# Performance work log

Measured on AMD Instinct MI355X. Metric: run time of the kernel, lower is better.

## Reference

```python
import jax, jax.numpy as jnp
import numpy as np

K = 3          # involution kernel size
GROUPS = 32    # channels == GROUPS * K*K
BN_EPS = 1e-5

def _conv1x1(x, W, b):
    # x: (B,C,H,W), W: (Co,C), b: (Co,)
    return jnp.einsum('bchw,oc->bohw', x, W) + b[None, :, None, None]

def setup_inputs() -> dict:
    key = jax.random.key(0)
    ks = jax.random.split(key, 5)
    C = GROUPS * K * K  # 288
    x = jax.random.normal(ks[0], (8, C, 64, 64), dtype=jnp.float32)
    Wi = jax.random.normal(ks[1], (C, C), dtype=jnp.float32) * 0.05
    bi = jnp.zeros((C,), dtype=jnp.float32)
    gamma = jnp.ones((C,), dtype=jnp.float32)
    beta = jnp.zeros((C,), dtype=jnp.float32)
    Wo = jax.random.normal(ks[2], (C, C), dtype=jnp.float32) * 0.05
    bo = jnp.zeros((C,), dtype=jnp.float32)
    return {"x": x, "Wi": Wi, "bi": bi, "gamma": gamma, "beta": beta, "Wo": Wo, "bo": bo}

def reference(x, Wi, bi, gamma, beta, Wo, bo):
    B, C, H, W = x.shape
    # kernel generation branch (stride=1 -> avgpool is identity)
    tmp = jax.nn.relu(_conv1x1(x, Wi, bi))
    # BatchNorm2d in training mode: batch stats over (N,H,W), biased variance
    mean = jnp.mean(tmp, axis=(0, 2, 3), keepdims=True)
    var = jnp.var(tmp, axis=(0, 2, 3), keepdims=True)
    tmp = (tmp - mean) * jax.lax.rsqrt(var + BN_EPS)
    tmp = tmp * gamma[None, :, None, None] + beta[None, :, None, None]
    ker = _conv1x1(tmp, Wo, bo)                       # (B, G*K^2, H, W)
    ker = ker.reshape(B, GROUPS, K * K, H, W)         # (B, G, K^2, H, W)
    # unfold: extract KxK patches with padding (K-1)//2, stride 1
    p = (K - 1) // 2
    xp = jnp.pad(x, ((0, 0), (0, 0), (p, p), (p, p)))
    patches = jnp.stack(
        [xp[:, :, i:i + H, j:j + W] for i in range(K) for j in range(K)],
        axis=2,
    )  # (B, C, K^2, H, W), kernel-position minor — matches torch unfold layout
    patches = patches.reshape(B, GROUPS, C // GROUPS, K * K, H, W)
    # per-pixel dynamic kernel multiply + sum over kernel positions
    out = jnp.einsum('bgkhw,bgckhw->bgchw', ker, patches)
    return out.reshape(B, C, H, W)
```

## Files before the change

### kernel.cpp

```cpp
#include <hip/hip_runtime.h>

#define CH   288
#define GRPS 32
#define CPG  9
#define IMH  64
#define IMW  64
#define HW   4096
#define NB   8
#define NPX  (NB * HW)
#define BN_EPS 1e-5f

typedef short bf16x8 __attribute__((ext_vector_type(8)));
typedef float f32x4  __attribute__((ext_vector_type(4)));

#define XT_OFF   0u
#define WIB_OFF  18874368u
#define WOS_OFF  19040256u
#define S1_OFF   19206144u
#define S2_OFF   19207296u
#define SC_OFF   19208448u
#define SH_OFF   19209600u
#define BO2_OFF  19210752u

#define XB 36864
#define WB 18432

__device__ __forceinline__ unsigned short f2b(float f) {
    unsigned int u = __float_as_uint(f);
    return (unsigned short)((u + 0x7fffu + ((u >> 16) & 1u)) >> 16);
}
__device__ __forceinline__ float b2f(unsigned short h) {
    return __uint_as_float(((unsigned int)h) << 16);
}

#define GLDS(g, l) __builtin_amdgcn_global_load_lds( \
    (const __attribute__((address_space(1))) void*)(g), \
    (__attribute__((address_space(3))) void*)(l), 16, 0, 0)

__device__ __forceinline__ f32x4 mfma16(bf16x8 a, bf16x8 b, f32x4 c) {
    return __builtin_amdgcn_mfma_f32_16x16x32_bf16(a, b, c, 0, 0, 0);
}

#define TS 40
__global__ __launch_bounds__(256) void k_transpose(const float* __restrict__ x,
                                                   unsigned short* __restrict__ xt) {
    __shared__ unsigned short T[64 * TS];
    const int tid = threadIdx.x;
    const int p0 = blockIdx.x * 64;
    const int c0 = blockIdx.y * 32;
    const int b  = blockIdx.z;
    #pragma unroll
    for (int it = 0; it < 2; ++it) {
        const int item  = it * 256 + tid;
        const int c_loc = item >> 4;
        const int p4    = item & 15;
        const float4 v = *(const float4*)(x + (size_t)(b * CH + c0 + c_loc) * HW + p0 + p4 * 4);
        const int px = p4 * 4;
        T[(px + 0) * TS + c_loc] = f2b(v.x);
        T[(px + 1) * TS + c_loc] = f2b(v.y);
        T[(px + 2) * TS + c_loc] = f2b(v.z);
        T[(px + 3) * TS + c_loc] = f2b(v.w);
    }
    __syncthreads();
    const int px_loc = tid >> 2;
    const int cq     = tid & 3;
    const uint4 o = *(const uint4*)((const char*)T + px_loc * (TS * 2) + cq * 16);
    *(uint4*)(xt + ((size_t)b * HW + p0 + px_loc) * CH + c0 + cq * 8) = o;
}

__global__ __launch_bounds__(256) void k_cvt_wi(const float* __restrict__ Wi,
                                                unsigned short* __restrict__ Wib) {
    const int idx = blockIdx.x * 256 + threadIdx.x;
    const float4 v = ((const float4*)Wi)[idx];
    unsigned short h[4] = {f2b(v.x), f2b(v.y), f2b(v.z), f2b(v.w)};
    *(uint2*)(Wib + (size_t)idx * 4) = *(const uint2*)h;
}

#define GEMM_STEP(KK, WBASE) do {                                              \
    bf16x8 xf0, xf1;                                                           \
    { const int row0 = pxh * 32 + r;                                           \
      xf0 = *(const bf16x8*)(smc + row0 * 576 + (KK) * 64 +                    \
                             ((q ^ ((row0 >> 1) & 3)) * 16)); }                \
    { const int row1 = pxh * 32 + 16 + r;                                      \
      xf1 = *(const bf16x8*)(smc + row1 * 576 + (KK) * 64 +                    \
                             ((q ^ ((row1 >> 1) & 3)) * 16)); }                \
    _Pragma("unroll")                                                          \
    for (int j = 0; j < 9; ++j) {                                              \
        const int ro = chh * 144 + j * 16 + r;                                 \
        const bf16x8 wf = *(const bf16x8*)((WBASE) + ro * 64 +                 \
                             ((q ^ ((ro >> 1) & 3)) * 16));                    \
        acc[0][j] = mfma16(wf, xf0, acc[0][j]);                                \
        acc[1][j] = mfma16(wf, xf1, acc[1][j]);                                \
    }                                                                          \
} while (0)

#define STAGE_W(WSRC, K0v, WDST) do {                                          \
    for (int s = wave; s < 18; s += 4) {                                       \
        const int row = s * 16 + lrow;                                         \
        const int sc  = lp ^ ((row >> 1) & 3);                                 \
        GLDS((WSRC) + (size_t)row * CH + (K0v) + sc * 8, (WDST) + s * 1024);   \
    }                                                                          \
} while (0)

#define STAGE_X(XSRC) do {                                                     \
    for (int s = wave; s < 36; s += 4) {                                       \
        const int d   = s * 1024 + lane * 16;                                  \
        const int px  = d / 576;                                               \
        const int rem = d - px * 576;                                          \
        const int kc  = rem >> 6;                                              \
        const int ch  = (rem >> 4) & 3;                                        \
        const int sc  = ch ^ ((px >> 1) & 3);                                  \
        GLDS((XSRC) + (size_t)px * CH + kc * 32 + sc * 8, smc + s * 1024);     \
    }                                                                          \
} while (0)

__global__ __launch_bounds__(256) void k_gemm1(const unsigned short* __restrict__ Wib,
                                               const float* __restrict__ bi,
                                               unsigned short* __restrict__ xt,
                                               float* __restrict__ s1g) {
    __shared__ char smc[XB + 2 * WB];

    const int tid  = threadIdx.x;
    const int wave = tid >> 6;
    const int lane = tid & 63;
    const int q    = lane >> 4;
    const int r    = lane & 15;
    const int pxh  = wave & 1;
    const int chh  = wave >> 1;
    const int p0   = blockIdx.x * 64;
    const int lrow = lane >> 2;
    const int lp   = lane & 3;

    f32x4 acc[2][9];
    #pragma unroll
    for (int t = 0; t < 2; ++t)
        #pragma unroll
        for (int j = 0; j < 9; ++j) acc[t][j] = (f32x4)0.0f;

    STAGE_X(xt + (size_t)p0 * CH);
    STAGE_W(Wib, 0, smc + XB);
    asm volatile("s_waitcnt vmcnt(0)" ::: "memory");
    __builtin_amdgcn_s_barrier();

    #pragma unroll 1
    for (int kk = 0; kk < 8; ++kk) {
        char* wnext = smc + XB + ((kk + 1) & 1) * WB;
        STAGE_W(Wib, (kk + 1) * 32, wnext);
        asm volatile("s_waitcnt vmcnt(4)" ::: "memory");
        __builtin_amdgcn_s_barrier();
        char* wcur = smc + XB + (kk & 1) * WB;
        GEMM_STEP(kk, wcur);
        __builtin_amdgcn_s_barrier();
    }
    asm volatile("s_waitcnt vmcnt(0)" ::: "memory");
    __builtin_amdgcn_s_barrier();
    GEMM_STEP(8, smc + XB);
    __syncthreads();

    float* sstat = (float*)(smc + 18432);
    for (int c2 = tid; c2 < 576; c2 += 256) sstat[c2] = 0.0f;
    __syncthreads();

    #pragma unroll 1
    for (int j = 0; j < 9; ++j) {
        const int cb = chh * 144 + j * 16 + q * 4;
        const float4 b4 = *(const float4*)(bi + cb);
        float a1[4] = {0.f, 0.f, 0.f, 0.f}, a2[4] = {0.f, 0.f, 0.f, 0.f};
        #pragma unroll
        for (int t = 0; t < 2; ++t) {
            float v0 = fmaxf(acc[t][j][0] + b4.x, 0.0f);
            float v1 = fmaxf(acc[t][j][1] + b4.y, 0.0f);
            float v2 = fmaxf(acc[t][j][2] + b4.z, 0.0f);
            float v3 = fmaxf(acc[t][j][3] + b4.w, 0.0f);
            a1[0] += v0; a1[1] += v1; a1[2] += v2; a1[3] += v3;
            a2[0] += v0 * v0; a2[1] += v1 * v1; a2[2] += v2 * v2; a2[3] += v3 * v3;
        }
        #pragma unroll
        for (int m = 1; m < 16; m <<= 1) {
            #pragma unroll
            for (int i = 0; i < 4; ++i) {
                a1[i] += __shfl_xor(a1[i], m, 64);
                a2[i] += __shfl_xor(a2[i], m, 64);
            }
        }
        if (r == 0) {
            #pragma unroll
            for (int i = 0; i < 4; ++i) {
                atomicAdd(&sstat[cb + i], a1[i]);
                atomicAdd(&sstat[288 + cb + i], a2[i]);
            }
        }
    }

    #pragma unroll
    for (int ph = 0; ph < 2; ++ph) {
        const int lr = pxh * 16 + r;
        #pragma unroll
        for (int j = 0; j < 9; ++j) {
            const int cb = chh * 144 + j * 16 + q * 4;
            const float4 b4 = *(const float4*)(bi + cb);
            unsigned short h[4];
            h[0] = f2b(fmaxf(acc[ph][j][0] + b4.x, 0.0f));
            h[1] = f2b(fmaxf(acc[ph][j][1] + b4.y, 0.0f));
            h[2] = f2b(fmaxf(acc[ph][j][2] + b4.z, 0.0f));
            h[3] = f2b(fmaxf(acc[ph][j][3] + b4.w, 0.0f));
            *(uint2*)(smc + lr * 576 + cb * 2) = *(const uint2*)h;
        }
        __syncthreads();
        for (int idx = tid; idx < 1152; idx += 256) {
            const int row = idx / 36;
            const int off = idx - row * 36;
            const int gpx = p0 + ph * 16 + row + (row & 16);
            *(uint4*)(xt + (size_t)gpx * CH + off * 8) =
                *(const uint4*)(smc + row * 576 + off * 16);
        }
        if (ph == 0) {
            for (int c2 = tid; c2 < 576; c2 += 256)
                atomicAdd(&s1g[c2], sstat[c2]);
        }
        __syncthreads();
    }
}

__global__ __launch_bounds__(320) void k_scale(const float* __restrict__ s1,
                                               const float* __restrict__ s2,
                                               const float* __restrict__ gamma,
                                               const float* __restrict__ beta,
                                               float* __restrict__ scale,
                                               float* __restrict__ shift) {
    const int c = threadIdx.x;
    if (c < CH) {
        const float inv = 1.0f / (float)(NB * HW);
        const float mean = s1[c] * inv;
        const float var  = s2[c] * inv - mean * mean;
        const float rs   = rsqrtf(var + BN_EPS);
        const float sc   = gamma[c] * rs;
        scale[c] = sc;
        shift[c] = beta[c] - mean * sc;
    }
}

__global__ __launch_bounds__(64) void k_fold(const float* __restrict__ Wo,
                                             const float* __restrict__ bo,
                                             const float* __restrict__ scale,
                                             const float* __restrict__ shift,
                                             unsigned short* __restrict__ Wos,
                                             float* __restrict__ bo2) {
    const int m = blockIdx.x;
    const int t = threadIdx.x;
    float s = 0.0f;
    for (int k = t; k < CH; k += 64) {
        const float wv = Wo[(size_t)m * CH + k];
        s += wv * shift[k];
        Wos[(size_t)m * CH + k] = f2b(wv * scale[k]);
    }
    #pragma unroll
    for (int off = 32; off > 0; off >>= 1) s += __shfl_down(s, off, 64);
    if (t == 0) bo2[m] = bo[m] + s;
}

#define KLS2 68
__global__ __launch_bounds__(256) void k_gemm2_invol(const unsigned short* __restrict__ xt,
                                                     const unsigned short* __restrict__ Wos,
                                                     const float* __restrict__ bo2,
                                                     const float* __restrict__ x,
                                                     float* __restrict__ out) {
    __shared__ char smc[XB + 2 * WB];
    unsigned short* kerL = (unsigned short*)smc;

    const int tid  = threadIdx.x;
    const int wave = tid >> 6;
    const int lane = tid & 63;
    const int q    = lane >> 4;
    const int r    = lane & 15;
    const int pxh  = wave & 1;
    const int chh  = wave >> 1;
    const int p0   = blockIdx.x * 64;
    const int b    = blockIdx.y;
    const int h    = blockIdx.x;
    const size_t rowbase = (size_t)b * HW + p0;
    const int lrow = lane >> 2;
    const int lp   = lane & 3;

    f32x4 acc[2][9];
    #pragma unroll
    for (int t = 0; t < 2; ++t)
        #pragma unroll
        for (int j = 0; j < 9; ++j) acc[t][j] = (f32x4)0.0f;

    STAGE_X(xt + rowbase * CH);
    STAGE_W(Wos, 0, smc + XB);
    asm volatile("s_waitcnt vmcnt(0)" ::: "memory");
    __builtin_amdgcn_s_barrier();

    #pragma unroll 1
    for (int kk = 0; kk < 8; ++kk) {
        char* wnext = smc + XB + ((kk + 1) & 1) * WB;
        STAGE_W(Wos, (kk + 1) * 32, wnext);
        asm volatile("s_waitcnt vmcnt(4)" ::: "memory");
        __builtin_amdgcn_s_barrier();
        char* wcur = smc + XB + (kk & 1) * WB;
        GEMM_STEP(kk, wcur);
        __builtin_amdgcn_s_barrier();
    }
    asm volatile("s_waitcnt vmcnt(0)" ::: "memory");
    __builtin_amdgcn_s_barrier();
    GEMM_STEP(8, smc + XB);
    __syncthreads();

    #pragma unroll
    for (int j = 0; j < 9; ++j) {
        const int cb = chh * 144 + j * 16 + q * 4;
        const float4 bz = *(const float4*)(bo2 + cb);
        #pragma unroll
        for (int t = 0; t < 2; ++t) {
            const int pxl = pxh * 32 + t * 16 + r;
            kerL[(cb + 0) * KLS2 + pxl] = f2b(acc[t][j][0] + bz.x);
            kerL[(cb + 1) * KLS2 + pxl] = f2b(acc[t][j][1] + bz.y);
            kerL[(cb + 2) * KLS2 + pxl] = f2b(acc[t][j][2] + bz.z);
            kerL[(cb + 3) * KLS2 + pxl] = f2b(acc[t][j][3] + bz.w);
        }
    }
    __syncthreads();

    const int tm = tid >> 4;
    const int tn = tid & 15;
    const int wb = tn * 4;
    #pragma unroll 1
    for (int i = 0; i < 18; ++i) {
        const int ch = tm + 16 * i;
        const int cb = (ch / CPG) * CPG;
        float xv[3][6];
        #pragma unroll
        for (int dr = 0; dr < 3; ++dr) {
            const int hh = h + dr - 1;
            const bool rv = (hh >= 0) && (hh < IMH);
            const float* xr2 = x + ((size_t)(b * CH + ch) * IMH + (rv ? hh : 0)) * IMW;
            if (rv) {
                const float4 m4 = *(const float4*)(xr2 + wb);
                xv[dr][1] = m4.x; xv[dr][2] = m4.y; xv[dr][3] = m4.z; xv[dr][4] = m4.w;
                xv[dr][0] = (wb > 0)       ? xr2[wb - 1] : 0.0f;
                xv[dr][5] = (wb + 4 < IMW) ? xr2[wb + 4] : 0.0f;
            } else {
                #pragma unroll
                for (int j = 0; j < 6; ++j) xv[dr][j] = 0.0f;
            }
        }
        float o[4] = {0.0f, 0.0f, 0.0f, 0.0f};
        #pragma unroll
        for (int k = 0; k < 9; ++k) {
            const int dr = k / 3, dc = k % 3;
            const uint2 kk = *(const uint2*)(kerL + (cb + k) * KLS2 + tn * 4);
            const unsigned short* ks = (const unsigned short*)&kk;
            #pragma unroll
            for (int j = 0; j < 4; ++j)
                o[j] += b2f(ks[j]) * xv[dr][j + dc];
        }
        float4 ov = {o[0], o[1], o[2], o[3]};
        *(float4*)(out + ((size_t)(b * CH + ch) * IMH + h) * IMW + wb) = ov;
    }
}

extern "C" void kernel_launch(void* const* d_in, const int* in_sizes, int n_in,
                              void* d_out, int out_size, void* d_ws, size_t ws_size,
                              hipStream_t stream) {
    const float* x     = (const float*)d_in[0];
    const float* Wi    = (const float*)d_in[1];
    const float* bi    = (const float*)d_in[2];
    const float* gamma = (const float*)d_in[3];
    const float* beta  = (const float*)d_in[4];
    const float* Wo    = (const float*)d_in[5];
    const float* bo    = (const float*)d_in[6];
    float* out = (float*)d_out;

    char* ws = (char*)d_ws;
    unsigned short* xt  = (unsigned short*)(ws + XT_OFF);
    unsigned short* Wib = (unsigned short*)(ws + WIB_OFF);
    unsigned short* Wos = (unsigned short*)(ws + WOS_OFF);
    float* s1    = (float*)(ws + S1_OFF);
    float* s2    = (float*)(ws + S2_OFF);
    float* scale = (float*)(ws + SC_OFF);
    float* shift = (float*)(ws + SH_OFF);
    float* bo2   = (float*)(ws + BO2_OFF);

    k_transpose<<<dim3(HW / 64, CH / 32, NB), 256, 0, stream>>>(x, xt);
    k_cvt_wi<<<dim3(CH * CH / 1024), 256, 0, stream>>>(Wi, Wib);
    hipMemsetAsync(ws + S1_OFF, 0, 2 * CH * sizeof(float), stream);
    k_gemm1<<<dim3(NPX / 64), 256, 0, stream>>>(Wib, bi, xt, s1);
    k_scale<<<dim3(1), 320, 0, stream>>>(s1, s2, gamma, beta, scale, shift);
    k_fold<<<dim3(CH), 64, 0, stream>>>(Wo, bo, scale, shift, Wos, bo2);
    k_gemm2_invol<<<dim3(HW / 64, NB), 256, 0, stream>>>(xt, Wos, bo2, x, out);
}
```

Before: 186.5 us.

## Shrink GEMM tiles, stream X with W per k-step, and spread BN-stat atomics over slots

gemm1 now processes 32 pixels per block instead of 64, with half the accumulators and launch_bounds(256,4), so more blocks can be resident per CU. Both GEMMs now stream X tiles k-slice by k-slice together with the weights instead of staging the full X tile up front, which shrinks LDS use. The global batch-norm atomics are spread over 64 slot buffers, which reuse the Wos workspace region, and k_scale reduces across the slots. This trades more blocks and extra X traffic per k-step for higher occupancy and less atomic contention, and it depends on k_fold overwriting the slot region afterwards.

```diff
diff --git a/kernel.cpp b/kernel.cpp
--- a/kernel.cpp
+++ b/kernel.cpp
@@ -9,6 +9,7 @@
 #define NB   8
 #define NPX  (NB * HW)
 #define BN_EPS 1e-5f
+#define NSLOT 64
 
 typedef short bf16x8 __attribute__((ext_vector_type(8)));
 typedef float f32x4  __attribute__((ext_vector_type(4)));
@@ -16,14 +17,12 @@
 #define XT_OFF   0u
 #define WIB_OFF  18874368u
 #define WOS_OFF  19040256u
-#define S1_OFF   19206144u
-#define S2_OFF   19207296u
 #define SC_OFF   19208448u
 #define SH_OFF   19209600u
 #define BO2_OFF  19210752u
 
-#define XB 36864
-#define WB 18432
+#define BUF1 20480
+#define BUF2 22528
 
 __device__ __forceinline__ unsigned short f2b(float f) {
     unsigned int u = __float_as_uint(f);
@@ -76,49 +75,11 @@
     *(uint2*)(Wib + (size_t)idx * 4) = *(const uint2*)h;
 }
 
-#define GEMM_STEP(KK, WBASE) do {                                              \
-    bf16x8 xf0, xf1;                                                           \
-    { const int row0 = pxh * 32 + r;                                           \
-      xf0 = *(const bf16x8*)(smc + row0 * 576 + (KK) * 64 +                    \
-                             ((q ^ ((row0 >> 1) & 3)) * 16)); }                \
-    { const int row1 = pxh * 32 + 16 + r;                                      \
-      xf1 = *(const bf16x8*)(smc + row1 * 576 + (KK) * 64 +                    \
-                             ((q ^ ((row1 >> 1) & 3)) * 16)); }                \
-    _Pragma("unroll")                                                          \
-    for (int j = 0; j < 9; ++j) {                                              \
-        const int ro = chh * 144 + j * 16 + r;                                 \
-        const bf16x8 wf = *(const bf16x8*)((WBASE) + ro * 64 +                 \
-                             ((q ^ ((ro >> 1) & 3)) * 16));                    \
-        acc[0][j] = mfma16(wf, xf0, acc[0][j]);                                \
-        acc[1][j] = mfma16(wf, xf1, acc[1][j]);                                \
-    }                                                                          \
-} while (0)
-
-#define STAGE_W(WSRC, K0v, WDST) do {                                          \
-    for (int s = wave; s < 18; s += 4) {                                       \
-        const int row = s * 16 + lrow;                                         \
-        const int sc  = lp ^ ((row >> 1) & 3);                                 \
-        GLDS((WSRC) + (size_t)row * CH + (K0v) + sc * 8, (WDST) + s * 1024);   \
-    }                                                                          \
-} while (0)
-
-#define STAGE_X(XSRC) do {                                                     \
-    for (int s = wave; s < 36; s += 4) {                                       \
-        const int d   = s * 1024 + lane * 16;                                  \
-        const int px  = d / 576;                                               \
-        const int rem = d - px * 576;                                          \
-        const int kc  = rem >> 6;                                              \
-        const int ch  = (rem >> 4) & 3;                                        \
-        const int sc  = ch ^ ((px >> 1) & 3);                                  \
-        GLDS((XSRC) + (size_t)px * CH + kc * 32 + sc * 8, smc + s * 1024);     \
-    }                                                                          \
-} while (0)
-
-__global__ __launch_bounds__(256) void k_gemm1(const unsigned short* __restrict__ Wib,
-                                               const float* __restrict__ bi,
-                                               unsigned short* __restrict__ xt,
-                                               float* __restrict__ s1g) {
-    __shared__ char smc[XB + 2 * WB];
+__global__ __launch_bounds__(256, 4) void k_gemm1(const unsigned short* __restrict__ Wib,
+                                                  const float* __restrict__ bi,
+                                                  unsigned short* __restrict__ xt,
+                                                  float* __restrict__ slots) {
+    __shared__ char smc[2 * BUF1];
 
     const int tid  = threadIdx.x;
     const int wave = tid >> 6;
@@ -127,37 +88,57 @@
     const int r    = lane & 15;
     const int pxh  = wave & 1;
     const int chh  = wave >> 1;
-    const int p0   = blockIdx.x * 64;
+    const int p0   = blockIdx.x * 32;
     const int lrow = lane >> 2;
     const int lp   = lane & 3;
 
-    f32x4 acc[2][9];
-    #pragma unroll
-    for (int t = 0; t < 2; ++t)
-        #pragma unroll
-        for (int j = 0; j < 9; ++j) acc[t][j] = (f32x4)0.0f;
-
-    STAGE_X(xt + (size_t)p0 * CH);
-    STAGE_W(Wib, 0, smc + XB);
+    f32x4 acc[9];
+    #pragma unroll
+    for (int j = 0; j < 9; ++j) acc[j] = (f32x4)0.0f;
+
+    const unsigned short* xsrc = xt + (size_t)p0 * CH;
+
+    #define STAGE1(K0v, DST) do {                                              \
+        for (int s = wave; s < 20; s += 4) {                                   \
+            const int row = s * 16 + lrow;                                     \
+            const int sc  = lp ^ ((row >> 1) & 3);                             \
+            const unsigned short* g = (s < 2)                                  \
+                ? xsrc + (size_t)row * CH + (K0v) + sc * 8                     \
+                : Wib  + (size_t)(row - 32) * CH + (K0v) + sc * 8;             \
+            GLDS(g, (DST) + s * 1024);                                         \
+        }                                                                      \
+    } while (0)
+
+    #define GSTEP1(BUF) do {                                                   \
+        const int xr = pxh * 16 + r;                                           \
+        const bf16x8 xf = *(const bf16x8*)((BUF) + xr * 64 +                   \
+                             ((q ^ ((xr >> 1) & 3)) * 16));                    \
+        _Pragma("unroll")                                                      \
+        for (int j = 0; j < 9; ++j) {                                          \
+            const int wr = 32 + chh * 144 + j * 16 + r;                        \
+            const bf16x8 wf = *(const bf16x8*)((BUF) + wr * 64 +               \
+                                 ((q ^ ((wr >> 1) & 3)) * 16));                \
+            acc[j] = mfma16(wf, xf, acc[j]);                                   \
+        }                                                                      \
+    } while (0)
+
+    STAGE1(0, smc);
     asm volatile("s_waitcnt vmcnt(0)" ::: "memory");
     __builtin_amdgcn_s_barrier();
-
     #pragma unroll 1
     for (int kk = 0; kk < 8; ++kk) {
-        char* wnext = smc + XB + ((kk + 1) & 1) * WB;
-        STAGE_W(Wib, (kk + 1) * 32, wnext);
-        asm volatile("s_waitcnt vmcnt(4)" ::: "memory");
+        STAGE1((kk + 1) * 32, smc + ((kk + 1) & 1) * BUF1);
+        asm volatile("s_waitcnt vmcnt(5)" ::: "memory");
         __builtin_amdgcn_s_barrier();
-        char* wcur = smc + XB + (kk & 1) * WB;
-        GEMM_STEP(kk, wcur);
+        GSTEP1(smc + (kk & 1) * BUF1);
         __builtin_amdgcn_s_barrier();
     }
     asm volatile("s_waitcnt vmcnt(0)" ::: "memory");
     __builtin_amdgcn_s_barrier();
-    GEMM_STEP(8, smc + XB);
-    __syncthreads();
-
-    float* sstat = (float*)(smc + 18432);
+    GSTEP1(smc);
+    __syncthreads();
+
+    float* sstat = (float*)(smc + 38656);
     for (int c2 = tid; c2 < 576; c2 += 256) sstat[c2] = 0.0f;
     __syncthreads();
 
@@ -165,16 +146,15 @@
     for (int j = 0; j < 9; ++j) {
         const int cb = chh * 144 + j * 16 + q * 4;
         const float4 b4 = *(const float4*)(bi + cb);
-        float a1[4] = {0.f, 0.f, 0.f, 0.f}, a2[4] = {0.f, 0.f, 0.f, 0.f};
-        #pragma unroll
-        for (int t = 0; t < 2; ++t) {
-            float v0 = fmaxf(acc[t][j][0] + b4.x, 0.0f);
-            float v1 = fmaxf(acc[t][j][1] + b4.y, 0.0f);
-            float v2 = fmaxf(acc[t][j][2] + b4.z, 0.0f);
-            float v3 = fmaxf(acc[t][j][3] + b4.w, 0.0f);
-            a1[0] += v0; a1[1] += v1; a1[2] += v2; a1[3] += v3;
-            a2[0] += v0 * v0; a2[1] += v1 * v1; a2[2] += v2 * v2; a2[3] += v3 * v3;
-        }
+        float v[4];
+        v[0] = fmaxf(acc[j][0] + b4.x, 0.0f);
+        v[1] = fmaxf(acc[j][1] + b4.y, 0.0f);
+        v[2] = fmaxf(acc[j][2] + b4.z, 0.0f);
+        v[3] = fmaxf(acc[j][3] + b4.w, 0.0f);
+        unsigned short h[4] = {f2b(v[0]), f2b(v[1]), f2b(v[2]), f2b(v[3])};
+        *(uint2*)(smc + (pxh * 16 + r) * 576 + cb * 2) = *(const uint2*)h;
+        float a1[4] = {v[0], v[1], v[2], v[3]};
+        float a2[4] = {v[0]*v[0], v[1]*v[1], v[2]*v[2], v[3]*v[3]};
         #pragma unroll
         for (int m = 1; m < 16; m <<= 1) {
             #pragma unroll
@@ -191,52 +171,39 @@
             }
         }
     }
-
-    #pragma unroll
-    for (int ph = 0; ph < 2; ++ph) {
-        const int lr = pxh * 16 + r;
-        #pragma unroll
-        for (int j = 0; j < 9; ++j) {
-            const int cb = chh * 144 + j * 16 + q * 4;
-            const float4 b4 = *(const float4*)(bi + cb);
-            unsigned short h[4];
-            h[0] = f2b(fmaxf(acc[ph][j][0] + b4.x, 0.0f));
-            h[1] = f2b(fmaxf(acc[ph][j][1] + b4.y, 0.0f));
-            h[2] = f2b(fmaxf(acc[ph][j][2] + b4.z, 0.0f));
-            h[3] = f2b(fmaxf(acc[ph][j][3] + b4.w, 0.0f));
-            *(uint2*)(smc + lr * 576 + cb * 2) = *(const uint2*)h;
-        }
-        __syncthreads();
-        for (int idx = tid; idx < 1152; idx += 256) {
-            const int row = idx / 36;
-            const int off = idx - row * 36;
-            const int gpx = p0 + ph * 16 + row + (row & 16);
-            *(uint4*)(xt + (size_t)gpx * CH + off * 8) =
-                *(const uint4*)(smc + row * 576 + off * 16);
-        }
-        if (ph == 0) {
-            for (int c2 = tid; c2 < 576; c2 += 256)
-                atomicAdd(&s1g[c2], sstat[c2]);
-        }
-        __syncthreads();
-    }
-}
-
-__global__ __launch_bounds__(320) void k_scale(const float* __restrict__ s1,
-                                               const float* __restrict__ s2,
+    __syncthreads();
+
+    for (int idx = tid; idx < 1152; idx += 256) {
+        const int row = idx / 36;
+        const int off = idx - row * 36;
+        *(uint4*)(xt + (size_t)(p0 + row) * CH + off * 8) =
+            *(const uint4*)(smc + row * 576 + off * 16);
+    }
+    float* slot = slots + (size_t)(blockIdx.x & (NSLOT - 1)) * 576;
+    for (int c2 = tid; c2 < 576; c2 += 256)
+        atomicAdd(&slot[c2], sstat[c2]);
+}
+
+__global__ __launch_bounds__(576) void k_scale(const float* __restrict__ slots,
                                                const float* __restrict__ gamma,
                                                const float* __restrict__ beta,
                                                float* __restrict__ scale,
                                                float* __restrict__ shift) {
-    const int c = threadIdx.x;
-    if (c < CH) {
-        const float inv = 1.0f / (float)(NB * HW);
-        const float mean = s1[c] * inv;
-        const float var  = s2[c] * inv - mean * mean;
+    __shared__ float red[576];
+    const int tid = threadIdx.x;
+    float s = 0.0f;
+    #pragma unroll 4
+    for (int sl = 0; sl < NSLOT; ++sl) s += slots[sl * 576 + tid];
+    red[tid] = s;
+    __syncthreads();
+    if (tid < CH) {
+        const float inv  = 1.0f / (float)(NB * HW);
+        const float mean = red[tid] * inv;
+        const float var  = red[288 + tid] * inv - mean * mean;
         const float rs   = rsqrtf(var + BN_EPS);
-        const float sc   = gamma[c] * rs;
-        scale[c] = sc;
-        shift[c] = beta[c] - mean * sc;
+        const float sc   = gamma[tid] * rs;
+        scale[tid] = sc;
+        shift[tid] = beta[tid] - mean * sc;
     }
 }
 
@@ -265,7 +232,7 @@
                                                      const float* __restrict__ bo2,
                                                      const float* __restrict__ x,
                                                      float* __restrict__ out) {
-    __shared__ char smc[XB + 2 * WB];
+    __shared__ char smc[2 * BUF2];
     unsigned short* kerL = (unsigned short*)smc;
 
     const int tid  = threadIdx.x;
@@ -288,24 +255,52 @@
         #pragma unroll
         for (int j = 0; j < 9; ++j) acc[t][j] = (f32x4)0.0f;
 
-    STAGE_X(xt + rowbase * CH);
-    STAGE_W(Wos, 0, smc + XB);
+    const unsigned short* xsrc = xt + rowbase * CH;
+
+    #define STAGE2(K0v, DST) do {                                              \
+        for (int s = wave; s < 22; s += 4) {                                   \
+            const int row = s * 16 + lrow;                                     \
+            const int sc  = lp ^ ((row >> 1) & 3);                             \
+            const unsigned short* g = (s < 4)                                  \
+                ? xsrc + (size_t)row * CH + (K0v) + sc * 8                     \
+                : Wos  + (size_t)(row - 64) * CH + (K0v) + sc * 8;             \
+            GLDS(g, (DST) + s * 1024);                                         \
+        }                                                                      \
+    } while (0)
+
+    #define GSTEP2(BUF) do {                                                   \
+        bf16x8 xf0, xf1;                                                       \
+        { const int xr = pxh * 32 + r;                                         \
+          xf0 = *(const bf16x8*)((BUF) + xr * 64 +                             \
+                     ((q ^ ((xr >> 1) & 3)) * 16)); }                          \
+        { const int xr = pxh * 32 + 16 + r;                                    \
+          xf1 = *(const bf16x8*)((BUF) + xr * 64 +                             \
+                     ((q ^ ((xr >> 1) & 3)) * 16)); }                          \
+        _Pragma("unroll")                                                      \
+        for (int j = 0; j < 9; ++j) {                                          \
+            const int wr = 64 + chh * 144 + j * 16 + r;                        \
+            const bf16x8 wf = *(const bf16x8*)((BUF) + wr * 64 +               \
+                                 ((q ^ ((wr >> 1) & 3)) * 16));                \
+            acc[0][j] = mfma16(wf, xf0, acc[0][j]);                            \
+            acc[1][j] = mfma16(wf, xf1, acc[1][j]);                            \
+        }                                                                      \
+    } while (0)
+
+    STAGE2(0, smc);
     asm volatile("s_waitcnt vmcnt(0)" ::: "memory");
     __builtin_amdgcn_s_barrier();
-
     #pragma unroll 1
     for (int kk = 0; kk < 8; ++kk) {
-        char* wnext = smc + XB + ((kk + 1) & 1) * WB;
-        STAGE_W(Wos, (kk + 1) * 32, wnext);
-        asm volatile("s_waitcnt vmcnt(4)" ::: "memory");
+        STAGE2((kk + 1) * 32, smc + ((kk + 1) & 1) * BUF2);
+        if (wave < 2) { asm volatile("s_waitcnt vmcnt(6)" ::: "memory"); }
+        else          { asm volatile("s_waitcnt vmcnt(5)" ::: "memory"); }
         __builtin_amdgcn_s_barrier();
-        char* wcur = smc + XB + (kk & 1) * WB;
-        GEMM_STEP(kk, wcur);
+        GSTEP2(smc + (kk & 1) * BUF2);
         __builtin_amdgcn_s_barrier();
     }
     asm volatile("s_waitcnt vmcnt(0)" ::: "memory");
     __builtin_amdgcn_s_barrier();
-    GEMM_STEP(8, smc + XB);
+    GSTEP2(smc);
     __syncthreads();
 
     #pragma unroll
@@ -377,17 +372,16 @@
     unsigned short* xt  = (unsigned short*)(ws + XT_OFF);
     unsigned short* Wib = (unsigned short*)(ws + WIB_OFF);
     unsigned short* Wos = (unsigned short*)(ws + WOS_OFF);
-    float* s1    = (float*)(ws + S1_OFF);
-    float* s2    = (float*)(ws + S2_OFF);
+    float* slots = (float*)(ws + WOS_OFF);
     float* scale = (float*)(ws + SC_OFF);
     float* shift = (float*)(ws + SH_OFF);
     float* bo2   = (float*)(ws + BO2_OFF);
 
     k_transpose<<<dim3(HW / 64, CH / 32, NB), 256, 0, stream>>>(x, xt);
     k_cvt_wi<<<dim3(CH * CH / 1024), 256, 0, stream>>>(Wi, Wib);
-    hipMemsetAsync(ws + S1_OFF, 0, 2 * CH * sizeof(float), stream);
-    k_gemm1<<<dim3(NPX / 64), 256, 0, stream>>>(Wib, bi, xt, s1);
-    k_scale<<<dim3(1), 320, 0, stream>>>(s1, s2, gamma, beta, scale, shift);
+    hipMemsetAsync(ws + WOS_OFF, 0, NSLOT * 576 * sizeof(float), stream);
+    k_gemm1<<<dim3(NPX / 32), 256, 0, stream>>>(Wib, bi, xt, slots);
+    k_scale<<<dim3(1), 576, 0, stream>>>(slots, gamma, beta, scale, shift);
     k_fold<<<dim3(CH), 64, 0, stream>>>(Wo, bo, scale, shift, Wos, bo2);
     k_gemm2_invol<<<dim3(HW / 64, NB), 256, 0, stream>>>(xt, Wos, bo2, x, out);
 }
```

Measured after the change: 187.9 us. Within noise of the previous version (+0.7%).
